# Performance work log

Hardware: AMD Instinct MI355X
Metric: run time of the kernel (lower is better)

## Reference

```python
import jax, jax.numpy as jnp
import numpy as np

B, H, W = 4, 64, 1024
h, w = 32, 512
K = 16
C = 64
EPS = 1e-5


def setup_inputs() -> dict:
    key = jax.random.key(0)
    ks = jax.random.split(key, 8)
    n_sampled = h * w
    xyz_proj = jax.random.normal(ks[0], (B, H, W, 3), dtype=jnp.float32)
    points_proj = jax.random.normal(ks[1], (B, H, W, C), dtype=jnp.float32)
    xyz_sampled_proj = jax.random.normal(ks[2], (B, h, w, 3), dtype=jnp.float32)
    # Precomputed neighbor selection (stand-in for fused_conv_random_k, which is
    # a non-differentiable custom CUDA op producing detached indices + mask).
    neighbor_idx = jax.random.randint(ks[3], (B, n_sampled * K), 0, H * W, dtype=jnp.int32)
    valid_mask = (jax.random.uniform(ks[4], (B, n_sampled, K, 1)) > 0.1).astype(jnp.float32)
    # 1x1 conv MLP params (torch Conv2d weight (out,in,1,1) stored here as (in,out))
    def mk(k, cin, cout):
        kw, = jax.random.split(k, 1)
        wgt = jax.random.normal(kw, (cin, cout), dtype=jnp.float32) * (1.0 / np.sqrt(cin))
        return wgt
    w0 = mk(ks[5], 3 + C, 64)
    w1 = mk(ks[6], 64, 64)
    w2 = mk(ks[7], 64, 128)
    z = lambda c: jnp.zeros((c,), jnp.float32)
    o = lambda c: jnp.ones((c,), jnp.float32)
    return dict(
        xyz_proj=xyz_proj, points_proj=points_proj, xyz_sampled_proj=xyz_sampled_proj,
        neighbor_idx=neighbor_idx, valid_mask=valid_mask,
        w0=w0, b0=z(64), g0=o(64), be0=z(64), m0=z(64), v0=o(64),
        w1=w1, b1=z(64), g1=o(64), be1=z(64), m1=z(64), v1=o(64),
        w2=w2, b2=z(128), g2=o(128), be2=z(128), m2=z(128), v2=o(128),
    )


def _conv_bn_relu(x, wgt, b, g, be, m, v):
    # 1x1 conv == matmul over channel dim; BN in eval mode with running stats.
    y = jnp.einsum('bnkc,co->bnko', x, wgt) + b
    y = g * (y - m) * jax.lax.rsqrt(v + EPS) + be
    return jax.nn.relu(y)


def reference(xyz_proj, points_proj, xyz_sampled_proj, neighbor_idx, valid_mask,
              w0, b0, g0, be0, m0, v0,
              w1, b1, g1, be1, m1, v1,
              w2, b2, g2, be2, m2, v2):
    Bc = xyz_proj.shape[0]
    Cc = points_proj.shape[3]
    hh, ww = xyz_sampled_proj.shape[1], xyz_sampled_proj.shape[2]
    n_sampled = hh * ww
    xyz_bn3 = xyz_proj.reshape(Bc, -1, 3)          # (B, H*W, 3)
    points_bnc = points_proj.reshape(Bc, -1, Cc)   # (B, H*W, C)
    idx = neighbor_idx[..., None]                  # (B, n*K, 1)
    new_xyz_group = jnp.take_along_axis(xyz_bn3, idx, axis=1).reshape(Bc, n_sampled, K, 3)
    new_points_group = jnp.take_along_axis(points_bnc, idx, axis=1).reshape(Bc, n_sampled, K, Cc)
    new_xyz_group = new_xyz_group * valid_mask
    new_points_group = new_points_group * valid_mask
    new_xyz = xyz_sampled_proj.reshape(Bc, n_sampled, 1, 3)
    xyz_diff = new_xyz_group - new_xyz             # broadcast over K
    feat = jnp.concatenate([xyz_diff, new_points_group], axis=-1)  # (B, n, K, 3+C)
    feat = _conv_bn_relu(feat, w0, b0, g0, be0, m0, v0)
    feat = _conv_bn_relu(feat, w1, b1, g1, be1, m1, v1)
    feat = _conv_bn_relu(feat, w2, b2, g2, be2, m2, v2)
    points_down_sample = jnp.max(feat, axis=2)     # (B, n, 128) max-pool over K
    points_down_sample_proj = points_down_sample.reshape(Bc, hh, ww, -1)
    return points_down_sample, points_down_sample_proj
```

## Files before the change

### kernel.cpp

```cpp
#include <hip/hip_runtime.h>


#define HW_      65536
#define NPT_     16384
#define OUTHALF_ 8388608
#define XS_      72
#define EPS_     1e-5f
#define GRID_    1024
#define NIT_     (NPT_ / GRID_)

typedef _Float16 h8    __attribute__((ext_vector_type(8)));
typedef float    f32x4 __attribute__((ext_vector_type(4)));

__global__ __launch_bounds__(256) void cvt_pts_kernel(
    const float* __restrict__ src, _Float16* __restrict__ dst)
{
    const size_t i = ((size_t)blockIdx.x * 256 + threadIdx.x) * 8;
    f32x4 a = *(const f32x4*)(src + i);
    f32x4 b = *(const f32x4*)(src + i + 4);
    h8 o;
#pragma unroll
    for (int j = 0; j < 4; ++j) { o[j] = (_Float16)a[j]; o[4 + j] = (_Float16)b[j]; }
    *(h8*)(dst + i) = o;
}

template<bool PRE>
__global__ __launch_bounds__(256, 2) void pnsa_main(
    const float* __restrict__ xyz,
    const void*  __restrict__ ptsv,
    const float* __restrict__ xyzs,
    const int*   __restrict__ nidx,
    const float* __restrict__ vmask,
    const float* __restrict__ w0, const float* __restrict__ b0,
    const float* __restrict__ g0, const float* __restrict__ be0,
    const float* __restrict__ m0, const float* __restrict__ v0,
    const float* __restrict__ w1, const float* __restrict__ b1,
    const float* __restrict__ g1, const float* __restrict__ be1,
    const float* __restrict__ m1, const float* __restrict__ v1,
    const float* __restrict__ w2, const float* __restrict__ b2,
    const float* __restrict__ g2, const float* __restrict__ be2,
    const float* __restrict__ m2, const float* __restrict__ v2,
    float*       __restrict__ out)
{
    __shared__ __align__(16) unsigned short ldsX1[4][16 * XS_];
    __shared__ __align__(16) unsigned short ldsX2[4][16 * XS_];

    const int tid  = threadIdx.x;
    const int wave = tid >> 6;
    const int lane = tid & 63;
    const int l15  = lane & 15;
    const int quad = lane >> 4;

    unsigned short* X1 = &ldsX1[wave][0];
    unsigned short* X2 = &ldsX2[wave][0];

    h8    b0f[4][3], b1f[4][2], b2f[8][2];
    float t0r[4], t1r[4], t2r[8];

#pragma unroll
    for (int nt = 0; nt < 4; ++nt) {
        const int ch = nt * 16 + l15;
        const float s = g0[ch] * rsqrtf(v0[ch] + EPS_);
        t0r[nt] = (b0[ch] - m0[ch]) * s + be0[ch];
#pragma unroll
        for (int kk = 0; kk < 3; ++kk) {
            h8 f;
#pragma unroll
            for (int j = 0; j < 8; ++j) {
                const int k = kk * 32 + quad * 8 + j;
                float wv = 0.f;
                if (k < 64)      wv = w0[(3 + k) * 64 + ch];
                else if (k < 67) wv = w0[(k - 64) * 64 + ch];
                f[j] = (_Float16)(wv * s);
            }
            b0f[nt][kk] = f;
        }
    }
#pragma unroll
    for (int nt = 0; nt < 4; ++nt) {
        const int ch = nt * 16 + l15;
        const float s = g1[ch] * rsqrtf(v1[ch] + EPS_);
        t1r[nt] = (b1[ch] - m1[ch]) * s + be1[ch];
#pragma unroll
        for (int kk = 0; kk < 2; ++kk) {
            h8 f;
#pragma unroll
            for (int j = 0; j < 8; ++j)
                f[j] = (_Float16)(w1[(kk * 32 + quad * 8 + j) * 64 + ch] * s);
            b1f[nt][kk] = f;
        }
    }
#pragma unroll
    for (int nt = 0; nt < 8; ++nt) {
        const int ch = nt * 16 + l15;
        const float s = g2[ch] * rsqrtf(v2[ch] + EPS_);
        t2r[nt] = (b2[ch] - m2[ch]) * s + be2[ch];
#pragma unroll
        for (int kk = 0; kk < 2; ++kk) {
            h8 f;
#pragma unroll
            for (int j = 0; j < 8; ++j)
                f[j] = (_Float16)(w2[(kk * 32 + quad * 8 + j) * 128 + ch] * s);
            b2f[nt][kk] = f;
        }
    }

    auto issue_pts = [&](int p_, int nb_, h8& q0, h8& q1,
                         float& xga, float& xgb, float& xgc) {
        const size_t row = (size_t)(((p_ >> 14) << 16) + nb_);
        if constexpr (PRE) {
            const _Float16* pw = (const _Float16*)ptsv + (row << 6);
            q0 = *(const h8*)(pw + quad * 8);
            q1 = *(const h8*)(pw + 32 + quad * 8);
        }
        const float* xgp = xyz + row * 3;
        xga = xgp[0]; xgb = xgp[1]; xgc = xgp[2];
    };
    auto issue_aux = [&](int p_, float& xsa, float& xsb, float& xsc, float& mk) {
        mk = vmask[(p_ << 4) + l15];
        const float* xsp = xyzs + (size_t)p_ * 3;
        xsa = xsp[0]; xsb = xsp[1]; xsc = xsp[2];
    };

    const int g = blockIdx.x;
    const int p0 = (g << 2) + wave;
    int nbc = nidx[(p0 << 4) + l15];
    h8 q0c, q1c;
    float xg0c, xg1c, xg2c, xs0c, xs1c, xs2c, mkc;
    issue_pts(p0, nbc, q0c, q1c, xg0c, xg1c, xg2c);
    issue_aux(p0, xs0c, xs1c, xs2c, mkc);
    const int g1i = (NIT_ > 1) ? g + GRID_ : g;
    int nbn = nidx[((((g1i << 2) + wave)) << 4) + l15];

    for (int it = 0; it < NIT_; ++it) {
        const int gcur = g + it * GRID_;
        const int pcur = (gcur << 2) + wave;
        const int gn   = (it + 1 < NIT_) ? gcur + GRID_ : gcur;
        const int pn   = (gn << 2) + wave;
        const int gn2  = (it + 2 < NIT_) ? gcur + 2 * GRID_ : gn;
        const int pn2  = (gn2 << 2) + wave;

        h8 q0n, q1n;
        float xg0n, xg1n, xg2n, xs0n, xs1n, xs2n, mkn;
        issue_pts(pn, nbn, q0n, q1n, xg0n, xg1n, xg2n);
        issue_aux(pn, xs0n, xs1n, xs2n, mkn);
        const int nbn2 = nidx[(pn2 << 4) + l15];

        h8 a0, a1, a2;
        if constexpr (PRE) {
            a0 = q0c; a1 = q1c;
        } else {
            const size_t row = (size_t)(((pcur >> 14) << 16) + nbc);
            const float* pw = (const float*)ptsv + (row << 6);
            f32x4 r0 = *(const f32x4*)(pw + quad * 8);
            f32x4 r1 = *(const f32x4*)(pw + quad * 8 + 4);
            f32x4 r2 = *(const f32x4*)(pw + 32 + quad * 8);
            f32x4 r3 = *(const f32x4*)(pw + 32 + quad * 8 + 4);
#pragma unroll
            for (int j = 0; j < 4; ++j) {
                a0[j] = (_Float16)r0[j]; a0[4 + j] = (_Float16)r1[j];
                a1[j] = (_Float16)r2[j]; a1[4 + j] = (_Float16)r3[j];
            }
        }
        if (mkc == 0.0f) { a0 = (h8)(_Float16)0.f; a1 = (h8)(_Float16)0.f; }
        a2 = (h8)(_Float16)0.f;
        if (quad == 0) {
            a2[0] = (_Float16)(xg0c * mkc - xs0c);
            a2[1] = (_Float16)(xg1c * mkc - xs1c);
            a2[2] = (_Float16)(xg2c * mkc - xs2c);
        }

#pragma unroll
        for (int nt = 0; nt < 4; ++nt) {
            f32x4 acc = {0.f, 0.f, 0.f, 0.f};
            acc = __builtin_amdgcn_mfma_f32_16x16x32_f16(a0, b0f[nt][0], acc, 0, 0, 0);
            acc = __builtin_amdgcn_mfma_f32_16x16x32_f16(a1, b0f[nt][1], acc, 0, 0, 0);
            acc = __builtin_amdgcn_mfma_f32_16x16x32_f16(a2, b0f[nt][2], acc, 0, 0, 0);
#pragma unroll
            for (int r = 0; r < 4; ++r) {
                const _Float16 hv = (_Float16)fmaxf(acc[r] + t0r[nt], 0.f);
                X1[(quad * 4 + r) * XS_ + nt * 16 + l15] = __builtin_bit_cast(unsigned short, hv);
            }
        }

        h8 x0 = *(const h8*)(X1 + l15 * XS_ + quad * 8);
        h8 x1 = *(const h8*)(X1 + l15 * XS_ + 32 + quad * 8);
#pragma unroll
        for (int nt = 0; nt < 4; ++nt) {
            f32x4 acc = {0.f, 0.f, 0.f, 0.f};
            acc = __builtin_amdgcn_mfma_f32_16x16x32_f16(x0, b1f[nt][0], acc, 0, 0, 0);
            acc = __builtin_amdgcn_mfma_f32_16x16x32_f16(x1, b1f[nt][1], acc, 0, 0, 0);
#pragma unroll
            for (int r = 0; r < 4; ++r) {
                const _Float16 hv = (_Float16)fmaxf(acc[r] + t1r[nt], 0.f);
                X2[(quad * 4 + r) * XS_ + nt * 16 + l15] = __builtin_bit_cast(unsigned short, hv);
            }
        }

        h8 y0 = *(const h8*)(X2 + l15 * XS_ + quad * 8);
        h8 y1 = *(const h8*)(X2 + l15 * XS_ + 32 + quad * 8);
        float rm[8];
#pragma unroll
        for (int nt = 0; nt < 8; ++nt) {
            f32x4 acc = {0.f, 0.f, 0.f, 0.f};
            acc = __builtin_amdgcn_mfma_f32_16x16x32_f16(y0, b2f[nt][0], acc, 0, 0, 0);
            acc = __builtin_amdgcn_mfma_f32_16x16x32_f16(y1, b2f[nt][1], acc, 0, 0, 0);
            float v = 0.f;
#pragma unroll
            for (int r = 0; r < 4; ++r) v = fmaxf(v, acc[r] + t2r[nt]);
            v = fmaxf(v, __shfl_xor(v, 16, 64));
            v = fmaxf(v, __shfl_xor(v, 32, 64));
            rm[nt] = v;
        }
        float* ob = out + ((size_t)pcur << 7);
#pragma unroll
        for (int ntg = 0; ntg < 2; ++ntg) {
            const float s01 = (quad == 0) ? rm[ntg * 4 + 0] : rm[ntg * 4 + 1];
            const float s23 = (quad == 2) ? rm[ntg * 4 + 2] : rm[ntg * 4 + 3];
            const float vv  = (quad < 2) ? s01 : s23;
            ob[ntg * 64 + lane]            = vv;
            ob[OUTHALF_ + ntg * 64 + lane] = vv;
        }

        nbc = nbn; nbn = nbn2;
        q0c = q0n; q1c = q1n;
        xg0c = xg0n; xg1c = xg1n; xg2c = xg2n;
        xs0c = xs0n; xs1c = xs1n; xs2c = xs2n;
        mkc = mkn;
    }
}

extern "C" void kernel_launch(void* const* d_in, const int* in_sizes, int n_in,
                              void* d_out, int out_size, void* d_ws, size_t ws_size,
                              hipStream_t stream) {
    const float* xyz   = (const float*)d_in[0];
    const float* pts   = (const float*)d_in[1];
    const float* xyzs  = (const float*)d_in[2];
    const int*   nidx  = (const int*)d_in[3];
    const float* vmask = (const float*)d_in[4];
    const float *w0 = (const float*)d_in[5],  *b0 = (const float*)d_in[6],
                *g0 = (const float*)d_in[7],  *be0 = (const float*)d_in[8],
                *m0 = (const float*)d_in[9],  *v0 = (const float*)d_in[10];
    const float *w1 = (const float*)d_in[11], *b1 = (const float*)d_in[12],
                *g1 = (const float*)d_in[13], *be1 = (const float*)d_in[14],
                *m1 = (const float*)d_in[15], *v1 = (const float*)d_in[16];
    const float *w2 = (const float*)d_in[17], *b2 = (const float*)d_in[18],
                *g2 = (const float*)d_in[19], *be2 = (const float*)d_in[20],
                *m2 = (const float*)d_in[21], *v2 = (const float*)d_in[22];
    float* outp = (float*)d_out;

    const size_t PTS_ELEMS = 16777216ull;
    if (ws_size >= PTS_ELEMS * sizeof(_Float16)) {
        _Float16* ptsh = (_Float16*)d_ws;
        cvt_pts_kernel<<<dim3(8192), dim3(256), 0, stream>>>(pts, ptsh);
        pnsa_main<true><<<dim3(GRID_), dim3(256), 0, stream>>>(
            xyz, (const void*)ptsh, xyzs, nidx, vmask,
            w0, b0, g0, be0, m0, v0,
            w1, b1, g1, be1, m1, v1,
            w2, b2, g2, be2, m2, v2, outp);
    } else {
        pnsa_main<false><<<dim3(GRID_), dim3(256), 0, stream>>>(
            xyz, (const void*)pts, xyzs, nidx, vmask,
            w0, b0, g0, be0, m0, v0,
            w1, b1, g1, be1, m1, v1,
            w2, b2, g2, be2, m2, v2, outp);
    }
}
```

Before: 231.7 us.

## Move layer-2 weights to LDS, fold layer-0 bias into MFMA, raise occupancy

The third-layer weight fragments, previously held in registers by every wave, are now staged once per block into padded shared memory and read per tile. The layer-0 bias is folded into the matmul by adding a constant-one input column, and the two per-wave activation buffers are merged into one. Together these cut register and LDS use so launch bounds can ask for three blocks per CU instead of two. The cost is extra LDS reads in the inner loop, plus a block-wide preload and sync, and fp16 rounding of the layer-0 bias.

```diff
diff --git a/kernel.cpp b/kernel.cpp
--- a/kernel.cpp
+++ b/kernel.cpp
@@ -1,10 +1,10 @@
 #include <hip/hip_runtime.h>
 
 
-#define HW_      65536
 #define NPT_     16384
 #define OUTHALF_ 8388608
 #define XS_      72
+#define W2S_     72
 #define EPS_     1e-5f
 #define GRID_    1024
 #define NIT_     (NPT_ / GRID_)
@@ -25,7 +25,7 @@
 }
 
 template<bool PRE>
-__global__ __launch_bounds__(256, 2) void pnsa_main(
+__global__ __launch_bounds__(256, 3) void pnsa_main(
     const float* __restrict__ xyz,
     const void*  __restrict__ ptsv,
     const float* __restrict__ xyzs,
@@ -42,8 +42,9 @@
     const float* __restrict__ m2, const float* __restrict__ v2,
     float*       __restrict__ out)
 {
-    __shared__ __align__(16) unsigned short ldsX1[4][16 * XS_];
-    __shared__ __align__(16) unsigned short ldsX2[4][16 * XS_];
+    __shared__ __align__(16) _Float16       ldsW2[128 * W2S_];
+    __shared__ __align__(16) float          s2sh[128];
+    __shared__ __align__(16) unsigned short ldsX[4][16 * XS_];
 
     const int tid  = threadIdx.x;
     const int wave = tid >> 6;
@@ -51,17 +52,28 @@
     const int l15  = lane & 15;
     const int quad = lane >> 4;
 
-    unsigned short* X1 = &ldsX1[wave][0];
-    unsigned short* X2 = &ldsX2[wave][0];
-
-    h8    b0f[4][3], b1f[4][2], b2f[8][2];
-    float t0r[4], t1r[4], t2r[8];
+    unsigned short* Xb = &ldsX[wave][0];
+
+    if (tid < 128) s2sh[tid] = g2[tid] * rsqrtf(v2[tid] + EPS_);
+    __syncthreads();
+    for (int idx = tid; idx < 64 * 128; idx += 256) {
+        const int k = idx >> 7, n = idx & 127;
+        ldsW2[n * W2S_ + k] = (_Float16)(w2[idx] * s2sh[n]);
+    }
+    for (int idx = tid; idx < 128 * 8; idx += 256) {
+        const int n = idx >> 3, k = 64 + (idx & 7);
+        ldsW2[n * W2S_ + k] = (_Float16)0.f;
+    }
+    __syncthreads();
+
+    h8    b0f[4][3], b1f[4][2];
+    float t1r[4], t2r[8];
 
 #pragma unroll
     for (int nt = 0; nt < 4; ++nt) {
         const int ch = nt * 16 + l15;
         const float s = g0[ch] * rsqrtf(v0[ch] + EPS_);
-        t0r[nt] = (b0[ch] - m0[ch]) * s + be0[ch];
+        const float t0 = (b0[ch] - m0[ch]) * s + be0[ch];
 #pragma unroll
         for (int kk = 0; kk < 3; ++kk) {
             h8 f;
@@ -69,9 +81,10 @@
             for (int j = 0; j < 8; ++j) {
                 const int k = kk * 32 + quad * 8 + j;
                 float wv = 0.f;
-                if (k < 64)      wv = w0[(3 + k) * 64 + ch];
-                else if (k < 67) wv = w0[(k - 64) * 64 + ch];
-                f[j] = (_Float16)(wv * s);
+                if (k < 64)       wv = w0[(3 + k) * 64 + ch] * s;
+                else if (k < 67)  wv = w0[(k - 64) * 64 + ch] * s;
+                else if (k == 67) wv = t0;
+                f[j] = (_Float16)wv;
             }
             b0f[nt][kk] = f;
         }
@@ -93,16 +106,7 @@
 #pragma unroll
     for (int nt = 0; nt < 8; ++nt) {
         const int ch = nt * 16 + l15;
-        const float s = g2[ch] * rsqrtf(v2[ch] + EPS_);
-        t2r[nt] = (b2[ch] - m2[ch]) * s + be2[ch];
-#pragma unroll
-        for (int kk = 0; kk < 2; ++kk) {
-            h8 f;
-#pragma unroll
-            for (int j = 0; j < 8; ++j)
-                f[j] = (_Float16)(w2[(kk * 32 + quad * 8 + j) * 128 + ch] * s);
-            b2f[nt][kk] = f;
-        }
+        t2r[nt] = (b2[ch] - m2[ch]) * s2sh[ch] + be2[ch];
     }
 
     auto issue_pts = [&](int p_, int nb_, h8& q0, h8& q1,
@@ -168,6 +172,7 @@
             a2[0] = (_Float16)(xg0c * mkc - xs0c);
             a2[1] = (_Float16)(xg1c * mkc - xs1c);
             a2[2] = (_Float16)(xg2c * mkc - xs2c);
+            a2[3] = (_Float16)1.0f;
         }
 
 #pragma unroll
@@ -178,13 +183,13 @@
             acc = __builtin_amdgcn_mfma_f32_16x16x32_f16(a2, b0f[nt][2], acc, 0, 0, 0);
 #pragma unroll
             for (int r = 0; r < 4; ++r) {
-                const _Float16 hv = (_Float16)fmaxf(acc[r] + t0r[nt], 0.f);
-                X1[(quad * 4 + r) * XS_ + nt * 16 + l15] = __builtin_bit_cast(unsigned short, hv);
-            }
-        }
-
-        h8 x0 = *(const h8*)(X1 + l15 * XS_ + quad * 8);
-        h8 x1 = *(const h8*)(X1 + l15 * XS_ + 32 + quad * 8);
+                const _Float16 hv = (_Float16)fmaxf(acc[r], 0.f);
+                Xb[(quad * 4 + r) * XS_ + nt * 16 + l15] = __builtin_bit_cast(unsigned short, hv);
+            }
+        }
+
+        h8 x0 = *(const h8*)(Xb + l15 * XS_ + quad * 8);
+        h8 x1 = *(const h8*)(Xb + l15 * XS_ + 32 + quad * 8);
 #pragma unroll
         for (int nt = 0; nt < 4; ++nt) {
             f32x4 acc = {0.f, 0.f, 0.f, 0.f};
@@ -193,18 +198,21 @@
 #pragma unroll
             for (int r = 0; r < 4; ++r) {
                 const _Float16 hv = (_Float16)fmaxf(acc[r] + t1r[nt], 0.f);
-                X2[(quad * 4 + r) * XS_ + nt * 16 + l15] = __builtin_bit_cast(unsigned short, hv);
-            }
-        }
-
-        h8 y0 = *(const h8*)(X2 + l15 * XS_ + quad * 8);
-        h8 y1 = *(const h8*)(X2 + l15 * XS_ + 32 + quad * 8);
+                Xb[(quad * 4 + r) * XS_ + nt * 16 + l15] = __builtin_bit_cast(unsigned short, hv);
+            }
+        }
+
+        h8 y0 = *(const h8*)(Xb + l15 * XS_ + quad * 8);
+        h8 y1 = *(const h8*)(Xb + l15 * XS_ + 32 + quad * 8);
         float rm[8];
 #pragma unroll
         for (int nt = 0; nt < 8; ++nt) {
+            const _Float16* wrow = ldsW2 + (nt * 16 + l15) * W2S_;
+            h8 wa = *(const h8*)(wrow + quad * 8);
+            h8 wb = *(const h8*)(wrow + 32 + quad * 8);
             f32x4 acc = {0.f, 0.f, 0.f, 0.f};
-            acc = __builtin_amdgcn_mfma_f32_16x16x32_f16(y0, b2f[nt][0], acc, 0, 0, 0);
-            acc = __builtin_amdgcn_mfma_f32_16x16x32_f16(y1, b2f[nt][1], acc, 0, 0, 0);
+            acc = __builtin_amdgcn_mfma_f32_16x16x32_f16(y0, wa, acc, 0, 0, 0);
+            acc = __builtin_amdgcn_mfma_f32_16x16x32_f16(y1, wb, acc, 0, 0, 0);
             float v = 0.f;
 #pragma unroll
             for (int r = 0; r < 4; ++r) v = fmaxf(v, acc[r] + t2r[nt]);
```

Result: slower. 371.1 us (+60.1%).
